# Optimization experiments

Hardware: AMD Instinct MI355X
Metric: run time of the kernel (lower is better)

The kernel has to match this reference:

```python
import jax, jax.numpy as jnp
import numpy as np

INPUT_DIM = 1024
HIDDEN_DIM = 1024


def setup_inputs() -> dict:
    key = jax.random.key(0)
    ks = jax.random.split(key, 7)
    B, S = 4, 2048
    s = 1.0 / np.sqrt(INPUT_DIM)
    x = jax.random.normal(ks[0], (B, S, INPUT_DIM), dtype=jnp.float32)
    Wq = jax.random.normal(ks[1], (HIDDEN_DIM, INPUT_DIM), dtype=jnp.float32) * s
    bq = jnp.zeros((HIDDEN_DIM,), dtype=jnp.float32)
    Wk = jax.random.normal(ks[2], (HIDDEN_DIM, INPUT_DIM), dtype=jnp.float32) * s
    bk = jnp.zeros((HIDDEN_DIM,), dtype=jnp.float32)
    Wv = jax.random.normal(ks[3], (HIDDEN_DIM, INPUT_DIM), dtype=jnp.float32) * s
    bv = jnp.zeros((HIDDEN_DIM,), dtype=jnp.float32)
    return {"x": x, "Wq": Wq, "bq": bq, "Wk": Wk, "bk": bk, "Wv": Wv, "bv": bv}


def reference(x, Wq, bq, Wk, bk, Wv, bv):
    # Linear layers: y = x @ W.T + b (torch nn.Linear convention)
    q = jnp.einsum('bsi,hi->bsh', x, Wq) + bq
    k = jnp.einsum('bsi,hi->bsh', x, Wk) + bk
    v = jnp.einsum('bsi,hi->bsh', x, Wv) + bv
    scale = 1.0 / jnp.sqrt(jnp.asarray(q.shape[-1], dtype=q.dtype))
    scores = jnp.einsum('bsh,bth->bst', q, k) * scale  # [B,S,S]
    attention_weights = jax.nn.softmax(scores, axis=-1)
    weighted_sum = jnp.einsum('bst,bth->bsh', attention_weights, v)
    return (weighted_sum, attention_weights)
```

## Files before the change

### kernel.cpp

```cpp
#include <hip/hip_runtime.h>
#include <hip/hip_bf16.h>
#include <cstdint>


typedef __bf16 bf16x8 __attribute__((ext_vector_type(8)));
typedef float  f32x4  __attribute__((ext_vector_type(4)));

__device__ __forceinline__ void load_lds16(const __bf16* g, __bf16* l) {
    __builtin_amdgcn_global_load_lds(
        (const __attribute__((address_space(1))) void*)g,
        (__attribute__((address_space(3))) void*)l,
        16, 0, 0);
}

__global__ __launch_bounds__(256) void cvt_f32_bf16(
        const float* __restrict__ src, __bf16* __restrict__ dst, int n8) {
    int i = blockIdx.x * blockDim.x + threadIdx.x;
    if (i >= n8) return;
    const float4* s4 = (const float4*)src;
    float4 a = s4[2 * i], b = s4[2 * i + 1];
    bf16x8 o;
    o[0] = (__bf16)a.x; o[1] = (__bf16)a.y; o[2] = (__bf16)a.z; o[3] = (__bf16)a.w;
    o[4] = (__bf16)b.x; o[5] = (__bf16)b.y; o[6] = (__bf16)b.z; o[7] = (__bf16)b.w;
    ((bf16x8*)dst)[i] = o;
}

template <int MODE>
__global__ __launch_bounds__(256, 2) void gemm_nt(
        const __bf16* __restrict__ A, const __bf16* __restrict__ Bt,
        void* __restrict__ Cout, const float* __restrict__ bias,
        int M, int N, int K, long sA, long sB, long sC, float scale) {
    __shared__ __bf16 lA[128 * 32];
    __shared__ __bf16 lB[128 * 32];

    const int tid  = threadIdx.x;
    const int lane = tid & 63;
    const int wave = tid >> 6;
    const int mblk = blockIdx.y * 128;
    const int nblk = blockIdx.x * 128;
    const int z    = blockIdx.z;
    A  += (long)z * sA;
    Bt += (long)z * sB;

    const int wm = (wave >> 1) * 64;
    const int wn = (wave & 1) * 64;

    f32x4 zero = {0.f, 0.f, 0.f, 0.f};
    f32x4 acc[4][4];
#pragma unroll
    for (int i = 0; i < 4; ++i)
#pragma unroll
        for (int j = 0; j < 4; ++j) acc[i][j] = zero;

    const int kq   = (lane >> 4) * 8;
    const int rsel = lane & 15;

    for (int k0 = 0; k0 < K; k0 += 32) {
#pragma unroll
        for (int it = 0; it < 2; ++it) {
            int c   = tid + it * 256;
            int row = c >> 2;
            int col = (c & 3) * 8;
            load_lds16(A  + (long)(mblk + row) * K + k0 + col, lA + c * 8);
            load_lds16(Bt + (long)(nblk + row) * K + k0 + col, lB + c * 8);
        }
        __syncthreads();

        bf16x8 fa[4], fb[4];
#pragma unroll
        for (int i = 0; i < 4; ++i) {
            fa[i] = *(const bf16x8*)&lA[(wm + i * 16 + rsel) * 32 + kq];
            fb[i] = *(const bf16x8*)&lB[(wn + i * 16 + rsel) * 32 + kq];
        }
#pragma unroll
        for (int i = 0; i < 4; ++i)
#pragma unroll
            for (int j = 0; j < 4; ++j)
                acc[i][j] = __builtin_amdgcn_mfma_f32_16x16x32_bf16(
                    fa[i], fb[j], acc[i][j], 0, 0, 0);
        __syncthreads();
    }

    const int rq = (lane >> 4) * 4;
#pragma unroll
    for (int i = 0; i < 4; ++i) {
#pragma unroll
        for (int j = 0; j < 4; ++j) {
            const int n = nblk + wn + j * 16 + rsel;
            if constexpr (MODE == 0) {
                __bf16* C = (__bf16*)Cout + (long)z * sC;
                float bv = bias[n];
#pragma unroll
                for (int r = 0; r < 4; ++r) {
                    int m = mblk + wm + i * 16 + rq + r;
                    C[(long)m * N + n] = (__bf16)(acc[i][j][r] + bv);
                }
            } else if constexpr (MODE == 1) {
                float* C = (float*)Cout + (long)z * sC;
#pragma unroll
                for (int r = 0; r < 4; ++r) {
                    int m = mblk + wm + i * 16 + rq + r;
                    C[(long)m * N + n] = acc[i][j][r] * scale;
                }
            } else {
                float* C = (float*)Cout + (long)z * sC;
#pragma unroll
                for (int r = 0; r < 4; ++r) {
                    int m = mblk + wm + i * 16 + rq + r;
                    C[(long)m * N + n] = acc[i][j][r];
                }
            }
        }
    }
}

__global__ __launch_bounds__(256) void softmax_rows(
        float* __restrict__ P, __bf16* __restrict__ Pb) {
    const long row = blockIdx.x;
    float*  p  = P  + row * 2048;
    __bf16* pb = Pb + row * 2048;
    const int tid  = threadIdx.x;
    const int lane = tid & 63;
    const int wave = tid >> 6;

    float4 v0 = ((const float4*)p)[tid * 2];
    float4 v1 = ((const float4*)p)[tid * 2 + 1];
    float e[8] = {v0.x, v0.y, v0.z, v0.w, v1.x, v1.y, v1.z, v1.w};

    float mx = e[0];
#pragma unroll
    for (int i = 1; i < 8; ++i) mx = fmaxf(mx, e[i]);
#pragma unroll
    for (int o = 1; o < 64; o <<= 1) mx = fmaxf(mx, __shfl_xor(mx, o, 64));

    __shared__ float redm[4], reds[4];
    if (lane == 0) redm[wave] = mx;
    __syncthreads();
    mx = fmaxf(fmaxf(redm[0], redm[1]), fmaxf(redm[2], redm[3]));

    float sum = 0.f;
#pragma unroll
    for (int i = 0; i < 8; ++i) { e[i] = __expf(e[i] - mx); sum += e[i]; }
#pragma unroll
    for (int o = 1; o < 64; o <<= 1) sum += __shfl_xor(sum, o, 64);
    if (lane == 0) reds[wave] = sum;
    __syncthreads();
    sum = reds[0] + reds[1] + reds[2] + reds[3];
    const float inv = 1.f / sum;

    float4 o0, o1;
    o0.x = e[0] * inv; o0.y = e[1] * inv; o0.z = e[2] * inv; o0.w = e[3] * inv;
    o1.x = e[4] * inv; o1.y = e[5] * inv; o1.z = e[6] * inv; o1.w = e[7] * inv;
    ((float4*)p)[tid * 2]     = o0;
    ((float4*)p)[tid * 2 + 1] = o1;
    bf16x8 ob;
    ob[0] = (__bf16)o0.x; ob[1] = (__bf16)o0.y; ob[2] = (__bf16)o0.z; ob[3] = (__bf16)o0.w;
    ob[4] = (__bf16)o1.x; ob[5] = (__bf16)o1.y; ob[6] = (__bf16)o1.z; ob[7] = (__bf16)o1.w;
    ((bf16x8*)pb)[tid] = ob;
}

__global__ __launch_bounds__(256) void transpose_v(
        const __bf16* __restrict__ src, __bf16* __restrict__ dst) {
    __shared__ __bf16 t[32][33];
    const int tx = threadIdx.x, ty = threadIdx.y;
    const int tileC = blockIdx.x * 32;
    const int tileR = blockIdx.y * 32;
    const long zs = (long)blockIdx.z * 2048 * 1024;
    const long zd = (long)blockIdx.z * 1024 * 2048;
#pragma unroll
    for (int k = 0; k < 4; ++k) {
        int r = ty * 4 + k;
        t[r][tx] = src[zs + (long)(tileR + r) * 1024 + tileC + tx];
    }
    __syncthreads();
#pragma unroll
    for (int k = 0; k < 4; ++k) {
        int c = ty * 4 + k;
        dst[zd + (long)(tileC + c) * 2048 + tileR + tx] = t[tx][c];
    }
}

extern "C" void kernel_launch(void* const* d_in, const int* in_sizes, int n_in,
                              void* d_out, int out_size, void* d_ws, size_t ws_size,
                              hipStream_t stream) {
    const float* x  = (const float*)d_in[0];
    const float* Wq = (const float*)d_in[1];
    const float* bq = (const float*)d_in[2];
    const float* Wk = (const float*)d_in[3];
    const float* bk = (const float*)d_in[4];
    const float* Wv = (const float*)d_in[5];
    const float* bv = (const float*)d_in[6];

    const int  S = 2048, H = 1024, I = 1024, B = 4;
    const long MS = (long)B * S;
    float* out_ws  = (float*)d_out;
    float* out_att = (float*)d_out + (long)B * S * H;

    char* w = (char*)d_ws;
    __bf16* x_bf  = (__bf16*)w; w += MS * I * 2;
    __bf16* wq_bf = (__bf16*)w; w += (long)H * I * 2;
    __bf16* wk_bf = (__bf16*)w; w += (long)H * I * 2;
    __bf16* wv_bf = (__bf16*)w; w += (long)H * I * 2;
    __bf16* q_bf  = (__bf16*)w; w += MS * H * 2;
    __bf16* k_bf  = (__bf16*)w; w += MS * H * 2;
    __bf16* v_bf  = (__bf16*)w; w += MS * H * 2;
    __bf16* vt_bf = (__bf16*)w; w += MS * H * 2;
    __bf16* p_bf  = (__bf16*)w; w += (long)B * S * S * 2;

    {
        int n8 = (int)(MS * I / 8);
        cvt_f32_bf16<<<dim3((n8 + 255) / 256), dim3(256), 0, stream>>>(x, x_bf, n8);
        int w8 = H * I / 8;
        cvt_f32_bf16<<<dim3((w8 + 255) / 256), dim3(256), 0, stream>>>(Wq, wq_bf, w8);
        cvt_f32_bf16<<<dim3((w8 + 255) / 256), dim3(256), 0, stream>>>(Wk, wk_bf, w8);
        cvt_f32_bf16<<<dim3((w8 + 255) / 256), dim3(256), 0, stream>>>(Wv, wv_bf, w8);
    }

    gemm_nt<0><<<dim3(8, 64, 1), dim3(256), 0, stream>>>(
        x_bf, wq_bf, q_bf, bq, 8192, 1024, 1024, 0, 0, 0, 1.f);
    gemm_nt<0><<<dim3(8, 64, 1), dim3(256), 0, stream>>>(
        x_bf, wk_bf, k_bf, bk, 8192, 1024, 1024, 0, 0, 0, 1.f);
    gemm_nt<0><<<dim3(8, 64, 1), dim3(256), 0, stream>>>(
        x_bf, wv_bf, v_bf, bv, 8192, 1024, 1024, 0, 0, 0, 1.f);

    transpose_v<<<dim3(32, 64, 4), dim3(32, 8), 0, stream>>>(v_bf, vt_bf);

    gemm_nt<1><<<dim3(16, 16, 4), dim3(256), 0, stream>>>(
        q_bf, k_bf, out_att, nullptr, 2048, 2048, 1024,
        (long)S * H, (long)S * H, (long)S * S, 0.03125f);

    softmax_rows<<<dim3(8192), dim3(256), 0, stream>>>(out_att, p_bf);

    gemm_nt<2><<<dim3(8, 16, 4), dim3(256), 0, stream>>>(
        p_bf, vt_bf, out_ws, nullptr, 2048, 1024, 2048,
        (long)S * S, (long)S * H, (long)S * H, 1.f);
}
```

Before: 361.6 us.

## Fuse QKV projections into one GEMM and use swizzled 64-deep K tiles

Packs Wq/Wk/Wv and biases into contiguous buffers so a single GEMM launch with N=3072 computes Q, K and V, routing each output column to its destination buffer. The GEMM K-step grows from 32 to 64 with an XOR-swizzled LDS layout meant to avoid bank conflicts, halving barrier count per K. Launch bounds are raised to 3 blocks per CU even though LDS per block doubles. This trades more LDS and register pressure for fewer launches, better fill of the GPU and fewer syncs.

```diff
diff --git a/kernel.cpp b/kernel.cpp
--- a/kernel.cpp
+++ b/kernel.cpp
@@ -25,13 +25,22 @@
     ((bf16x8*)dst)[i] = o;
 }
 
+__global__ __launch_bounds__(256) void pack_bias3(
+        const float* __restrict__ a, const float* __restrict__ b,
+        const float* __restrict__ c, float* __restrict__ o) {
+    int i = blockIdx.x * blockDim.x + threadIdx.x;
+    if (i < 1024) { o[i] = a[i]; o[i + 1024] = b[i]; o[i + 2048] = c[i]; }
+}
+
 template <int MODE>
-__global__ __launch_bounds__(256, 2) void gemm_nt(
+__global__ __launch_bounds__(256, 3) void gemm_nt(
         const __bf16* __restrict__ A, const __bf16* __restrict__ Bt,
-        void* __restrict__ Cout, const float* __restrict__ bias,
-        int M, int N, int K, long sA, long sB, long sC, float scale) {
-    __shared__ __bf16 lA[128 * 32];
-    __shared__ __bf16 lB[128 * 32];
+        void* __restrict__ C0, void* __restrict__ C1, void* __restrict__ C2,
+        const float* __restrict__ bias,
+        int lda, int ldb, int ldc, long sA, long sB, long sC,
+        int K, float scale) {
+    __shared__ __bf16 lA[128 * 64];
+    __shared__ __bf16 lB[128 * 64];
 
     const int tid  = threadIdx.x;
     const int lane = tid & 63;
@@ -52,62 +61,76 @@
 #pragma unroll
         for (int j = 0; j < 4; ++j) acc[i][j] = zero;
 
-    const int kq   = (lane >> 4) * 8;
     const int rsel = lane & 15;
-
-    for (int k0 = 0; k0 < K; k0 += 32) {
-#pragma unroll
-        for (int it = 0; it < 2; ++it) {
-            int c   = tid + it * 256;
-            int row = c >> 2;
-            int col = (c & 3) * 8;
-            load_lds16(A  + (long)(mblk + row) * K + k0 + col, lA + c * 8);
-            load_lds16(Bt + (long)(nblk + row) * K + k0 + col, lB + c * 8);
+    const int quad = lane >> 4;
+
+    int srow[4], scol[4];
+#pragma unroll
+    for (int it = 0; it < 4; ++it) {
+        int s  = tid + it * 256;
+        srow[it] = s >> 3;
+        scol[it] = ((s & 7) ^ (srow[it] & 7)) * 8;
+    }
+
+    for (int k0 = 0; k0 < K; k0 += 64) {
+#pragma unroll
+        for (int it = 0; it < 4; ++it) {
+            int s = tid + it * 256;
+            load_lds16(A  + (long)(mblk + srow[it]) * lda + k0 + scol[it], lA + s * 8);
+            load_lds16(Bt + (long)(nblk + srow[it]) * ldb + k0 + scol[it], lB + s * 8);
         }
         __syncthreads();
 
-        bf16x8 fa[4], fb[4];
-#pragma unroll
-        for (int i = 0; i < 4; ++i) {
-            fa[i] = *(const bf16x8*)&lA[(wm + i * 16 + rsel) * 32 + kq];
-            fb[i] = *(const bf16x8*)&lB[(wn + i * 16 + rsel) * 32 + kq];
+#pragma unroll
+        for (int half = 0; half < 2; ++half) {
+            const int cq = quad + half * 4;
+            bf16x8 fa[4], fb[4];
+#pragma unroll
+            for (int i = 0; i < 4; ++i) {
+                int ra = wm + i * 16 + rsel;
+                fa[i] = *(const bf16x8*)&lA[(ra * 8 + (cq ^ (ra & 7))) * 8];
+                int rb = wn + i * 16 + rsel;
+                fb[i] = *(const bf16x8*)&lB[(rb * 8 + (cq ^ (rb & 7))) * 8];
+            }
+#pragma unroll
+            for (int i = 0; i < 4; ++i)
+#pragma unroll
+                for (int j = 0; j < 4; ++j)
+                    acc[i][j] = __builtin_amdgcn_mfma_f32_16x16x32_bf16(
+                        fa[i], fb[j], acc[i][j], 0, 0, 0);
         }
-#pragma unroll
-        for (int i = 0; i < 4; ++i)
-#pragma unroll
-            for (int j = 0; j < 4; ++j)
-                acc[i][j] = __builtin_amdgcn_mfma_f32_16x16x32_bf16(
-                    fa[i], fb[j], acc[i][j], 0, 0, 0);
         __syncthreads();
     }
 
-    const int rq = (lane >> 4) * 4;
+    const int rq = quad * 4;
 #pragma unroll
     for (int i = 0; i < 4; ++i) {
 #pragma unroll
         for (int j = 0; j < 4; ++j) {
             const int n = nblk + wn + j * 16 + rsel;
             if constexpr (MODE == 0) {
-                __bf16* C = (__bf16*)Cout + (long)z * sC;
+                __bf16* C = (n < 1024) ? (__bf16*)C0
+                          : (n < 2048) ? (__bf16*)C1 : (__bf16*)C2;
+                const int col = n & 1023;
                 float bv = bias[n];
 #pragma unroll
                 for (int r = 0; r < 4; ++r) {
                     int m = mblk + wm + i * 16 + rq + r;
-                    C[(long)m * N + n] = (__bf16)(acc[i][j][r] + bv);
+                    C[(long)m * ldc + col] = (__bf16)(acc[i][j][r] + bv);
                 }
             } else if constexpr (MODE == 1) {
-                float* C = (float*)Cout + (long)z * sC;
+                float* C = (float*)C0 + (long)z * sC;
 #pragma unroll
                 for (int r = 0; r < 4; ++r) {
                     int m = mblk + wm + i * 16 + rq + r;
-                    C[(long)m * N + n] = acc[i][j][r] * scale;
+                    C[(long)m * ldc + n] = acc[i][j][r] * scale;
                 }
             } else {
-                float* C = (float*)Cout + (long)z * sC;
+                float* C = (float*)C0 + (long)z * sC;
 #pragma unroll
                 for (int r = 0; r < 4; ++r) {
                     int m = mblk + wm + i * 16 + rq + r;
-                    C[(long)m * N + n] = acc[i][j][r];
+                    C[(long)m * ldc + n] = acc[i][j][r];
                 }
             }
         }
@@ -197,41 +220,38 @@
     float* out_att = (float*)d_out + (long)B * S * H;
 
     char* w = (char*)d_ws;
-    __bf16* x_bf  = (__bf16*)w; w += MS * I * 2;
-    __bf16* wq_bf = (__bf16*)w; w += (long)H * I * 2;
-    __bf16* wk_bf = (__bf16*)w; w += (long)H * I * 2;
-    __bf16* wv_bf = (__bf16*)w; w += (long)H * I * 2;
-    __bf16* q_bf  = (__bf16*)w; w += MS * H * 2;
-    __bf16* k_bf  = (__bf16*)w; w += MS * H * 2;
-    __bf16* v_bf  = (__bf16*)w; w += MS * H * 2;
-    __bf16* vt_bf = (__bf16*)w; w += MS * H * 2;
-    __bf16* p_bf  = (__bf16*)w; w += (long)B * S * S * 2;
+    __bf16* x_bf   = (__bf16*)w; w += MS * I * 2;
+    __bf16* wqkv   = (__bf16*)w; w += (long)3 * H * I * 2;
+    float*  bias3  = (float*)w;  w += 4096 * 4;
+    __bf16* q_bf   = (__bf16*)w; w += MS * H * 2;
+    __bf16* k_bf   = (__bf16*)w; w += MS * H * 2;
+    __bf16* v_bf   = (__bf16*)w; w += MS * H * 2;
+    __bf16* vt_bf  = (__bf16*)w; w += MS * H * 2;
+    __bf16* p_bf   = (__bf16*)w; w += (long)B * S * S * 2;
 
     {
         int n8 = (int)(MS * I / 8);
         cvt_f32_bf16<<<dim3((n8 + 255) / 256), dim3(256), 0, stream>>>(x, x_bf, n8);
         int w8 = H * I / 8;
-        cvt_f32_bf16<<<dim3((w8 + 255) / 256), dim3(256), 0, stream>>>(Wq, wq_bf, w8);
-        cvt_f32_bf16<<<dim3((w8 + 255) / 256), dim3(256), 0, stream>>>(Wk, wk_bf, w8);
-        cvt_f32_bf16<<<dim3((w8 + 255) / 256), dim3(256), 0, stream>>>(Wv, wv_bf, w8);
-    }
-
-    gemm_nt<0><<<dim3(8, 64, 1), dim3(256), 0, stream>>>(
-        x_bf, wq_bf, q_bf, bq, 8192, 1024, 1024, 0, 0, 0, 1.f);
-    gemm_nt<0><<<dim3(8, 64, 1), dim3(256), 0, stream>>>(
-        x_bf, wk_bf, k_bf, bk, 8192, 1024, 1024, 0, 0, 0, 1.f);
-    gemm_nt<0><<<dim3(8, 64, 1), dim3(256), 0, stream>>>(
-        x_bf, wv_bf, v_bf, bv, 8192, 1024, 1024, 0, 0, 0, 1.f);
+        cvt_f32_bf16<<<dim3((w8 + 255) / 256), dim3(256), 0, stream>>>(Wq, wqkv, w8);
+        cvt_f32_bf16<<<dim3((w8 + 255) / 256), dim3(256), 0, stream>>>(Wk, wqkv + (long)H * I, w8);
+        cvt_f32_bf16<<<dim3((w8 + 255) / 256), dim3(256), 0, stream>>>(Wv, wqkv + (long)2 * H * I, w8);
+        pack_bias3<<<dim3(4), dim3(256), 0, stream>>>(bq, bk, bv, bias3);
+    }
+
+    gemm_nt<0><<<dim3(24, 64, 1), dim3(256), 0, stream>>>(
+        x_bf, wqkv, q_bf, k_bf, v_bf, bias3,
+        1024, 1024, 1024, 0, 0, 0, 1024, 1.f);
 
     transpose_v<<<dim3(32, 64, 4), dim3(32, 8), 0, stream>>>(v_bf, vt_bf);
 
     gemm_nt<1><<<dim3(16, 16, 4), dim3(256), 0, stream>>>(
-        q_bf, k_bf, out_att, nullptr, 2048, 2048, 1024,
-        (long)S * H, (long)S * H, (long)S * S, 0.03125f);
+        q_bf, k_bf, out_att, nullptr, nullptr, nullptr,
+        1024, 1024, 2048, (long)S * H, (long)S * H, (long)S * S, 1024, 0.03125f);
 
     softmax_rows<<<dim3(8192), dim3(256), 0, stream>>>(out_att, p_bf);
 
     gemm_nt<2><<<dim3(8, 16, 4), dim3(256), 0, stream>>>(
-        p_bf, vt_bf, out_ws, nullptr, 2048, 1024, 2048,
-        (long)S * S, (long)S * H, (long)S * H, 1.f);
-}
+        p_bf, vt_bf, out_ws, nullptr, nullptr, nullptr,
+        2048, 2048, 1024, (long)S * S, (long)S * H, (long)S * H, 2048, 1.f);
+}
```

Measured after the change: 318.1 us. 12.0% less time.
